# Optimization experiments

Hardware: AMD Instinct MI355X
Metric: run time of the kernel (lower is better)

Reference implementation:

```python
import jax, jax.numpy as jnp
import numpy as np

T, B = 2048, 64
E, H = 256, 256
VOCAB = 50257
PAD_ID = 0


def setup_inputs() -> dict:
    key = jax.random.key(0)
    ks = jax.random.split(key, 9)
    s = 0.05
    return {
        "sentences": jax.random.randint(ks[0], (T, B), 0, VOCAB, dtype=jnp.int64 if jax.config.jax_enable_x64 else jnp.int32),
        "noise": jax.random.uniform(ks[1], (T, B), dtype=jnp.float32),
        "emb": jax.random.normal(ks[2], (VOCAB, E), dtype=jnp.float32) * s,
        "W_ih": jax.random.normal(ks[3], (4 * H, E), dtype=jnp.float32) * s,
        "W_hh": jax.random.normal(ks[4], (4 * H, H), dtype=jnp.float32) * s,
        "b_ih": jax.random.normal(ks[5], (4 * H,), dtype=jnp.float32) * s,
        "b_hh": jax.random.normal(ks[6], (4 * H,), dtype=jnp.float32) * s,
        "W_z": jax.random.normal(ks[7], (H,), dtype=jnp.float32) * s,
        "b_z": jax.random.normal(ks[8], (), dtype=jnp.float32) * s,
    }


def _lstm(x, W_ih, W_hh, b_ih, b_hh):
    # x: (T, B, E) -> hidden states (T, B, H). PyTorch gate order: i, f, g, o.
    Hd = W_hh.shape[1]
    h0 = jnp.zeros((x.shape[1], Hd), x.dtype)
    c0 = jnp.zeros((x.shape[1], Hd), x.dtype)
    b = b_ih + b_hh

    def step(carry, x_t):
        h, c = carry
        g = x_t @ W_ih.T + h @ W_hh.T + b  # (B, 4H)
        i, f, gg, o = jnp.split(g, 4, axis=-1)
        c = jax.nn.sigmoid(f) * c + jax.nn.sigmoid(i) * jnp.tanh(gg)
        h = jax.nn.sigmoid(o) * jnp.tanh(c)
        return (h, c), h

    _, hs = jax.lax.scan(step, (h0, c0), x)
    return hs


def reference(sentences, noise, emb, W_ih, W_hh, b_ih, b_hh, W_z, b_z):
    x = emb[sentences]                         # (T, B, E) embedding gather
    hs = _lstm(x, W_ih, W_hh, b_ih, b_hh)      # (T, B, H)
    pz = jax.nn.sigmoid(jnp.einsum("tbh,h->tb", hs, W_z) + b_z)  # (T, B)
    z = (noise < pz).astype(pz.dtype)          # Bernoulli sample via uniform noise
    z_sizes = z.sum(axis=0).astype(jnp.int32)  # (B,)
    # Stream compaction per column: stable sort brings z==1 positions first,
    # preserving original token order (parallel equivalent of masked_select loop).
    order = jnp.argsort((1.0 - z).astype(jnp.int32), axis=0, stable=True)  # (T, B)
    selected = jnp.take_along_axis(sentences, order.astype(sentences.dtype), axis=0)
    pos = jnp.arange(sentences.shape[0])[:, None]
    rationales = jnp.where(pos < z_sizes[None, :], selected,
                           jnp.asarray(PAD_ID, sentences.dtype))
    return (pz, z, rationales, z_sizes)
```

## Files before the change

### kernel.cpp

```cpp
#include <hip/hip_runtime.h>
#include <math.h>

#define TT 2048
#define NB 64
#define EE 256
#define HH 256
#define PJ 16
#define XLD 288
#define RS1 280
#define RS2 72
#define RBOFF (8 * RS1)

typedef float f32x4 __attribute__((ext_vector_type(4)));

__device__ __forceinline__ float sigf(float x) { return 1.f / (1.f + expf(-x)); }

__device__ __forceinline__ unsigned long long packh(unsigned tag, float v) {
    union { float f; unsigned u; } c; c.f = v;
    return ((unsigned long long)tag << 32) | (unsigned long long)c.u;
}

__global__ __launch_bounds__(512, 2)
void lstm_kernel(const int* __restrict__ sent, const float* __restrict__ emb,
                 const float* __restrict__ W_ih, const float* __restrict__ W_hh,
                 const float* __restrict__ b_ih, const float* __restrict__ b_hh,
                 const float* __restrict__ W_z,
                 unsigned long long* __restrict__ hbuf,
                 float* __restrict__ part)
{
    __shared__ __align__(16) float x_sw[4 * XLD];
    __shared__ __align__(16) float h_sw[4 * XLD];
    __shared__ __align__(16) float red_s[2 * 8 * RS1];
    __shared__ __align__(16) float p_s[64];
    extern __shared__ float dyn_pad[];

    const int tid  = threadIdx.x;
    if (tid == 0 && sent[0] < 0) ((volatile float*)dyn_pad)[0] = 0.f;

    const int xcd  = blockIdx.x & 7;
    const int slot = blockIdx.x >> 3;
    const int psys = xcd * 2 + (slot >> 4);
    const int js   = slot & 15;
    const int bA0  = psys * 2;
    const int bB0  = 32 + psys * 2;
    const int j0   = js * 16;

    const int wv    = tid >> 6;
    const int lane  = tid & 63;
    const int bp    = wv & 1;
    const int kc    = (wv >> 1) * 2 + (lane & 1);
    const int rg    = lane >> 1;
    const int kbase = kc << 5;

    float4 wih_r[16], whh_r[16];
    #pragma unroll
    for (int i = 0; i < 2; ++i) {
        int lr = rg * 2 + i;
        long grow = (long)((lr >> 4) * HH + j0 + (lr & 15));
        const float4* wi = (const float4*)(W_ih + grow * EE + kbase);
        const float4* wh = (const float4*)(W_hh + grow * EE + kbase);
        #pragma unroll
        for (int mi = 0; mi < 8; ++mi) {
            wih_r[i * 8 + mi] = wi[mi];
            whh_r[i * 8 + mi] = wh[mi];
        }
    }

    const int eb  = (lane >> 4) & 1;
    const int ejj = lane & 15;
    float bias_g[4]; float wz_r = 0.f; float c_reg = 0.f;
    if (wv < 2) {
        #pragma unroll
        for (int g = 0; g < 4; ++g)
            bias_g[g] = b_ih[g * HH + j0 + ejj] + b_hh[g * HH + j0 + ejj];
        wz_r = W_z[j0 + ejj];
    }

    const bool spinA = (wv < 4);
    const bool spinB = (wv >= 4);
    const int sidx = ((wv & 3) << 6) + lane;
    const int scb  = sidx >> 7;
    const int scw  = (sidx & 127) << 1;
    const int scph = scw + ((scw >> 5) << 2);

    const bool stgA = (wv == 4 || wv == 5);
    const int srow  = (wv >= 6 ? 2 : 0) + bp;
    const int sphys = 4 * lane + ((lane >> 3) << 2);
    int tok_st = 0;

    if (wv >= 4) {
        int base = stgA ? bA0 : bB0;
        int tk0 = sent[0 * NB + base + bp];
        f32x4 xv0 = ((const f32x4*)(emb + (long)tk0 * EE))[lane];
        *(f32x4*)(&x_sw[srow * XLD + sphys]) = xv0;
        tok_st = sent[1 * NB + base + bp];
    }
    __syncthreads();

    for (int t = 0; t < TT; ++t) {
        const bool pf = (t + 1 < TT);
        const size_t parIn  = (size_t)(((t - 1) & 1) * NB);
        const size_t parOut = (size_t)((t & 1) * NB);
        const unsigned want = (unsigned)t;

        f32x4 xst;
        if (wv >= 4 && pf) {
            xst = ((const f32x4*)(emb + (long)tok_st * EE))[lane];
            if (t + 2 < TT)
                tok_st = sent[(t + 2) * NB + (stgA ? bA0 : bB0) + bp];
        }
        unsigned long long v0 = 0, v1 = 0;
        unsigned long long* hpA = hbuf + (parIn + bA0 + scb) * HH + scw;
        unsigned long long* hpB = hbuf + (parIn + bB0 + scb) * HH + scw;
        if (t > 0 && spinA) {
            v0 = __hip_atomic_load(hpA + 0, __ATOMIC_RELAXED, __HIP_MEMORY_SCOPE_AGENT);
            v1 = __hip_atomic_load(hpA + 1, __ATOMIC_RELAXED, __HIP_MEMORY_SCOPE_AGENT);
        }

        float4 acc[2];
        acc[0] = make_float4(0.f, 0.f, 0.f, 0.f);
        acc[1] = make_float4(0.f, 0.f, 0.f, 0.f);
        {
            const float* xb = &x_sw[bp * XLD + kc * 36];
            #pragma unroll
            for (int mi = 0; mi < 8; ++mi) {
                float4 xv4 = *(const float4*)(xb + mi * 4);
                #pragma unroll
                for (int i = 0; i < 2; ++i) {
                    float4 w = wih_r[i * 8 + mi];
                    acc[i].x += w.x * xv4.x; acc[i].y += w.y * xv4.y;
                    acc[i].z += w.z * xv4.z; acc[i].w += w.w * xv4.w;
                }
            }
        }
        if (t > 0 && spinA) {
            while ((unsigned)(v0 >> 32) != want)
                v0 = __hip_atomic_load(hpA + 0, __ATOMIC_RELAXED, __HIP_MEMORY_SCOPE_AGENT);
            while ((unsigned)(v1 >> 32) != want)
                v1 = __hip_atomic_load(hpA + 1, __ATOMIC_RELAXED, __HIP_MEMORY_SCOPE_AGENT);
            union { unsigned u; float f; } c0, c1;
            c0.u = (unsigned)v0; c1.u = (unsigned)v1;
            *(float2*)(&h_sw[scb * XLD + scph]) = make_float2(c0.f, c1.f);
        }
        __syncthreads();

        if (t > 0 && wv == 2 && lane < 2) {
            float s = 0.f;
            #pragma unroll
            for (int jj = 0; jj < 16; ++jj) s += p_s[lane * 16 + jj];
            part[((size_t)(t - 1) * PJ + js) * NB + bA0 + lane] = s;
        }
        if (t > 0 && spinB) {
            v0 = __hip_atomic_load(hpB + 0, __ATOMIC_RELAXED, __HIP_MEMORY_SCOPE_AGENT);
            v1 = __hip_atomic_load(hpB + 1, __ATOMIC_RELAXED, __HIP_MEMORY_SCOPE_AGENT);
        }
        if (t > 0) {
            const float* hb = &h_sw[bp * XLD + kc * 36];
            #pragma unroll
            for (int mi = 0; mi < 8; ++mi) {
                float4 hv4 = *(const float4*)(hb + mi * 4);
                #pragma unroll
                for (int i = 0; i < 2; ++i) {
                    float4 w = whh_r[i * 8 + mi];
                    acc[i].x += w.x * hv4.x; acc[i].y += w.y * hv4.y;
                    acc[i].z += w.z * hv4.z; acc[i].w += w.w * hv4.w;
                }
            }
        }
        {
            float2 v;
            v.x = (acc[0].x + acc[0].y) + (acc[0].z + acc[0].w);
            v.y = (acc[1].x + acc[1].y) + (acc[1].z + acc[1].w);
            *(float2*)(&red_s[kc * RS1 + bp * RS2 + rg * 2]) = v;
        }
        if (stgA && pf) {
            *(f32x4*)(&x_sw[srow * XLD + sphys]) = xst;
        }
        __syncthreads();

        if (wv == 0 && lane < 32) {
            float sg[4];
            #pragma unroll
            for (int g = 0; g < 4; ++g) {
                float s = bias_g[g];
                #pragma unroll
                for (int k2 = 0; k2 < 8; ++k2)
                    s += red_s[k2 * RS1 + eb * RS2 + g * 16 + ejj];
                sg[g] = s;
            }
            float cn = sigf(sg[1]) * c_reg + sigf(sg[0]) * tanhf(sg[2]);
            float hn = sigf(sg[3]) * tanhf(cn);
            c_reg = cn;
            p_s[lane] = hn * wz_r;
            __hip_atomic_store(
                hbuf + (parOut + bA0 + eb) * HH + j0 + ejj,
                packh((unsigned)(t + 1), hn),
                __ATOMIC_RELAXED, __HIP_MEMORY_SCOPE_AGENT);
        }

        acc[0] = make_float4(0.f, 0.f, 0.f, 0.f);
        acc[1] = make_float4(0.f, 0.f, 0.f, 0.f);
        {
            const float* xb = &x_sw[(2 + bp) * XLD + kc * 36];
            #pragma unroll
            for (int mi = 0; mi < 8; ++mi) {
                float4 xv4 = *(const float4*)(xb + mi * 4);
                #pragma unroll
                for (int i = 0; i < 2; ++i) {
                    float4 w = wih_r[i * 8 + mi];
                    acc[i].x += w.x * xv4.x; acc[i].y += w.y * xv4.y;
                    acc[i].z += w.z * xv4.z; acc[i].w += w.w * xv4.w;
                }
            }
        }
        if (t > 0 && spinB) {
            while ((unsigned)(v0 >> 32) != want)
                v0 = __hip_atomic_load(hpB + 0, __ATOMIC_RELAXED, __HIP_MEMORY_SCOPE_AGENT);
            while ((unsigned)(v1 >> 32) != want)
                v1 = __hip_atomic_load(hpB + 1, __ATOMIC_RELAXED, __HIP_MEMORY_SCOPE_AGENT);
            union { unsigned u; float f; } c0, c1;
            c0.u = (unsigned)v0; c1.u = (unsigned)v1;
            *(float2*)(&h_sw[(2 + scb) * XLD + scph]) = make_float2(c0.f, c1.f);
        }
        __syncthreads();

        if (t > 0 && wv == 3 && lane < 2) {
            float s = 0.f;
            #pragma unroll
            for (int jj = 0; jj < 16; ++jj) s += p_s[32 + lane * 16 + jj];
            part[((size_t)(t - 1) * PJ + js) * NB + bB0 + lane] = s;
        }
        if (t > 0) {
            const float* hb = &h_sw[(2 + bp) * XLD + kc * 36];
            #pragma unroll
            for (int mi = 0; mi < 8; ++mi) {
                float4 hv4 = *(const float4*)(hb + mi * 4);
                #pragma unroll
                for (int i = 0; i < 2; ++i) {
                    float4 w = whh_r[i * 8 + mi];
                    acc[i].x += w.x * hv4.x; acc[i].y += w.y * hv4.y;
                    acc[i].z += w.z * hv4.z; acc[i].w += w.w * hv4.w;
                }
            }
        }
        {
            float2 v;
            v.x = (acc[0].x + acc[0].y) + (acc[0].z + acc[0].w);
            v.y = (acc[1].x + acc[1].y) + (acc[1].z + acc[1].w);
            *(float2*)(&red_s[RBOFF + kc * RS1 + bp * RS2 + rg * 2]) = v;
        }
        if (!stgA && wv >= 4 && pf) {
            *(f32x4*)(&x_sw[srow * XLD + sphys]) = xst;
        }
        __syncthreads();

        if (wv == 1 && lane < 32) {
            float sg[4];
            #pragma unroll
            for (int g = 0; g < 4; ++g) {
                float s = bias_g[g];
                #pragma unroll
                for (int k2 = 0; k2 < 8; ++k2)
                    s += red_s[RBOFF + k2 * RS1 + eb * RS2 + g * 16 + ejj];
                sg[g] = s;
            }
            float cn = sigf(sg[1]) * c_reg + sigf(sg[0]) * tanhf(sg[2]);
            float hn = sigf(sg[3]) * tanhf(cn);
            c_reg = cn;
            p_s[32 + lane] = hn * wz_r;
            __hip_atomic_store(
                hbuf + (parOut + bB0 + eb) * HH + j0 + ejj,
                packh((unsigned)(t + 1), hn),
                __ATOMIC_RELAXED, __HIP_MEMORY_SCOPE_AGENT);
        }
    }

    __syncthreads();
    if (wv == 2 && lane < 2) {
        float s = 0.f;
        #pragma unroll
        for (int jj = 0; jj < 16; ++jj) s += p_s[lane * 16 + jj];
        part[((size_t)(TT - 1) * PJ + js) * NB + bA0 + lane] = s;
    }
    if (wv == 3 && lane < 2) {
        float s = 0.f;
        #pragma unroll
        for (int jj = 0; jj < 16; ++jj) s += p_s[32 + lane * 16 + jj];
        part[((size_t)(TT - 1) * PJ + js) * NB + bB0 + lane] = s;
    }
}

__global__ void pz_kernel(const float* __restrict__ part,
                          const float* __restrict__ noise,
                          const float* __restrict__ b_z,
                          float* __restrict__ out)
{
    int idx = blockIdx.x * blockDim.x + threadIdx.x;
    if (idx >= TT * NB) return;
    int t = idx >> 6, b = idx & 63;
    float s = b_z[0];
    #pragma unroll
    for (int jg = 0; jg < PJ; ++jg) s += part[(t * PJ + jg) * NB + b];
    float pz = 1.f / (1.f + expf(-s));
    out[idx] = pz;
    out[TT * NB + idx] = (noise[idx] < pz) ? 1.f : 0.f;
}

__global__ void compact_kernel(const int* __restrict__ sent,
                               const float* __restrict__ zbuf,
                               float* __restrict__ rat,
                               float* __restrict__ zsz)
{
    __shared__ float rat_s[TT];
    __shared__ int scan_s[256];
    int b = blockIdx.x, tid = threadIdx.x;
    int zloc[8];
    int base = tid * 8;
    int c = 0;
    #pragma unroll
    for (int i = 0; i < 8; ++i) {
        zloc[i] = (zbuf[(base + i) * NB + b] != 0.f) ? 1 : 0;
        c += zloc[i];
    }
    scan_s[tid] = c;
    for (int i = tid; i < TT; i += 256) rat_s[i] = 0.f;
    __syncthreads();
    for (int off = 1; off < 256; off <<= 1) {
        int v = scan_s[tid];
        int add = (tid >= off) ? scan_s[tid - off] : 0;
        __syncthreads();
        scan_s[tid] = v + add;
        __syncthreads();
    }
    int total = scan_s[255];
    int pos = scan_s[tid] - c;
    #pragma unroll
    for (int i = 0; i < 8; ++i) {
        if (zloc[i]) { rat_s[pos] = (float)sent[(base + i) * NB + b]; ++pos; }
    }
    __syncthreads();
    for (int i = tid; i < TT; i += 256) rat[i * NB + b] = rat_s[i];
    if (tid == 0) zsz[b] = (float)total;
}

extern "C" void kernel_launch(void* const* d_in, const int* in_sizes, int n_in,
                              void* d_out, int out_size, void* d_ws, size_t ws_size,
                              hipStream_t stream)
{
    const int*   sent  = (const int*)d_in[0];
    const float* noise = (const float*)d_in[1];
    const float* emb   = (const float*)d_in[2];
    const float* W_ih  = (const float*)d_in[3];
    const float* W_hh  = (const float*)d_in[4];
    const float* b_ih  = (const float*)d_in[5];
    const float* b_hh  = (const float*)d_in[6];
    const float* W_z   = (const float*)d_in[7];
    const float* b_z   = (const float*)d_in[8];
    float* out = (float*)d_out;

    char* ws = (char*)d_ws;
    unsigned long long* hbuf = (unsigned long long*)ws;
    float* part = (float*)(ws + 262144);

    (void)hipMemsetAsync(hbuf, 0, 2 * NB * HH * sizeof(unsigned long long), stream);

    lstm_kernel<<<256, 512, 65536, stream>>>(sent, emb, W_ih, W_hh, b_ih, b_hh,
                                             W_z, hbuf, part);
    pz_kernel<<<(TT * NB) / 256, 256, 0, stream>>>(part, noise, b_z, out);
    compact_kernel<<<NB, 256, 0, stream>>>(sent, out + TT * NB,
                                           out + 2 * TT * NB, out + 3 * TT * NB);
}
```

Baseline: 5.281 ms.

## Remove mid-phase barriers by having each wave poll its own hidden slice

Each wave now spin-loads only the h values it consumes (its kc slice for its batch row) and writes them into its own region of shared memory, so the separate poll-then-__syncthreads stage before each recurrent matvec is removed. This cuts the per-step barrier count from four to two. The B-group embedding staging buffer is double-buffered by timestep parity so it can be written without an extra barrier. The trade-off is that every wave now waits on remote atomics, and each wave issues scalar per-lane polls and shared stores instead of the earlier float2 pattern.

New measurement: 4.288 ms. 1.23x faster.

```diff
diff --git a/kernel.cpp b/kernel.cpp
--- a/kernel.cpp
+++ b/kernel.cpp
@@ -28,7 +28,7 @@
                  unsigned long long* __restrict__ hbuf,
                  float* __restrict__ part)
 {
-    __shared__ __align__(16) float x_sw[4 * XLD];
+    __shared__ __align__(16) float x_sw[6 * XLD];
     __shared__ __align__(16) float h_sw[4 * XLD];
     __shared__ __align__(16) float red_s[2 * 8 * RS1];
     __shared__ __align__(16) float p_s[64];
@@ -76,23 +76,20 @@
         wz_r = W_z[j0 + ejj];
     }
 
-    const bool spinA = (wv < 4);
-    const bool spinB = (wv >= 4);
-    const int sidx = ((wv & 3) << 6) + lane;
-    const int scb  = sidx >> 7;
-    const int scw  = (sidx & 127) << 1;
-    const int scph = scw + ((scw >> 5) << 2);
+    const int pj    = (kc << 5) + (lane >> 1);
+    const int pphys = kc * 36 + (lane >> 1);
 
     const bool stgA = (wv == 4 || wv == 5);
-    const int srow  = (wv >= 6 ? 2 : 0) + bp;
+    const bool stgB = (wv == 6 || wv == 7);
     const int sphys = 4 * lane + ((lane >> 3) << 2);
     int tok_st = 0;
 
-    if (wv >= 4) {
+    if (stgA || stgB) {
         int base = stgA ? bA0 : bB0;
         int tk0 = sent[0 * NB + base + bp];
         f32x4 xv0 = ((const f32x4*)(emb + (long)tk0 * EE))[lane];
-        *(f32x4*)(&x_sw[srow * XLD + sphys]) = xv0;
+        int row = stgA ? bp : (2 + bp);
+        *(f32x4*)(&x_sw[row * XLD + sphys]) = xv0;
         tok_st = sent[1 * NB + base + bp];
     }
     __syncthreads();
@@ -104,17 +101,21 @@
         const unsigned want = (unsigned)t;
 
         f32x4 xst;
-        if (wv >= 4 && pf) {
+        if ((stgA || stgB) && pf) {
             xst = ((const f32x4*)(emb + (long)tok_st * EE))[lane];
             if (t + 2 < TT)
                 tok_st = sent[(t + 2) * NB + (stgA ? bA0 : bB0) + bp];
         }
-        unsigned long long v0 = 0, v1 = 0;
-        unsigned long long* hpA = hbuf + (parIn + bA0 + scb) * HH + scw;
-        unsigned long long* hpB = hbuf + (parIn + bB0 + scb) * HH + scw;
-        if (t > 0 && spinA) {
-            v0 = __hip_atomic_load(hpA + 0, __ATOMIC_RELAXED, __HIP_MEMORY_SCOPE_AGENT);
-            v1 = __hip_atomic_load(hpA + 1, __ATOMIC_RELAXED, __HIP_MEMORY_SCOPE_AGENT);
+        unsigned long long* hpA = hbuf + (parIn + bA0 + bp) * HH + pj;
+        unsigned long long pv = 0;
+        if (t > 0)
+            pv = __hip_atomic_load(hpA, __ATOMIC_RELAXED, __HIP_MEMORY_SCOPE_AGENT);
+
+        if (t > 0 && wv == 2 && lane < 2) {
+            float s = 0.f;
+            #pragma unroll
+            for (int jj = 0; jj < 16; ++jj) s += p_s[lane * 16 + jj];
+            part[((size_t)(t - 1) * PJ + js) * NB + bA0 + lane] = s;
         }
 
         float4 acc[2];
@@ -133,28 +134,11 @@
                 }
             }
         }
-        if (t > 0 && spinA) {
-            while ((unsigned)(v0 >> 32) != want)
-                v0 = __hip_atomic_load(hpA + 0, __ATOMIC_RELAXED, __HIP_MEMORY_SCOPE_AGENT);
-            while ((unsigned)(v1 >> 32) != want)
-                v1 = __hip_atomic_load(hpA + 1, __ATOMIC_RELAXED, __HIP_MEMORY_SCOPE_AGENT);
-            union { unsigned u; float f; } c0, c1;
-            c0.u = (unsigned)v0; c1.u = (unsigned)v1;
-            *(float2*)(&h_sw[scb * XLD + scph]) = make_float2(c0.f, c1.f);
-        }
-        __syncthreads();
-
-        if (t > 0 && wv == 2 && lane < 2) {
-            float s = 0.f;
-            #pragma unroll
-            for (int jj = 0; jj < 16; ++jj) s += p_s[lane * 16 + jj];
-            part[((size_t)(t - 1) * PJ + js) * NB + bA0 + lane] = s;
-        }
-        if (t > 0 && spinB) {
-            v0 = __hip_atomic_load(hpB + 0, __ATOMIC_RELAXED, __HIP_MEMORY_SCOPE_AGENT);
-            v1 = __hip_atomic_load(hpB + 1, __ATOMIC_RELAXED, __HIP_MEMORY_SCOPE_AGENT);
-        }
         if (t > 0) {
+            while ((unsigned)(pv >> 32) != want)
+                pv = __hip_atomic_load(hpA, __ATOMIC_RELAXED, __HIP_MEMORY_SCOPE_AGENT);
+            union { unsigned u; float f; } cu; cu.u = (unsigned)pv;
+            h_sw[bp * XLD + pphys] = cu.f;
             const float* hb = &h_sw[bp * XLD + kc * 36];
             #pragma unroll
             for (int mi = 0; mi < 8; ++mi) {
@@ -173,10 +157,12 @@
             v.y = (acc[1].x + acc[1].y) + (acc[1].z + acc[1].w);
             *(float2*)(&red_s[kc * RS1 + bp * RS2 + rg * 2]) = v;
         }
-        if (stgA && pf) {
-            *(f32x4*)(&x_sw[srow * XLD + sphys]) = xst;
-        }
         __syncthreads();
+
+        unsigned long long* hpB = hbuf + (parIn + bB0 + bp) * HH + pj;
+        unsigned long long qv = 0;
+        if (t > 0)
+            qv = __hip_atomic_load(hpB, __ATOMIC_RELAXED, __HIP_MEMORY_SCOPE_AGENT);
 
         if (wv == 0 && lane < 32) {
             float sg[4];
@@ -197,11 +183,17 @@
                 packh((unsigned)(t + 1), hn),
                 __ATOMIC_RELAXED, __HIP_MEMORY_SCOPE_AGENT);
         }
+        if (t > 0 && wv == 3 && lane < 2) {
+            float s = 0.f;
+            #pragma unroll
+            for (int jj = 0; jj < 16; ++jj) s += p_s[32 + lane * 16 + jj];
+            part[((size_t)(t - 1) * PJ + js) * NB + bB0 + lane] = s;
+        }
 
         acc[0] = make_float4(0.f, 0.f, 0.f, 0.f);
         acc[1] = make_float4(0.f, 0.f, 0.f, 0.f);
         {
-            const float* xb = &x_sw[(2 + bp) * XLD + kc * 36];
+            const float* xb = &x_sw[(2 + 2 * (t & 1) + bp) * XLD + kc * 36];
             #pragma unroll
             for (int mi = 0; mi < 8; ++mi) {
                 float4 xv4 = *(const float4*)(xb + mi * 4);
@@ -213,24 +205,11 @@
                 }
             }
         }
-        if (t > 0 && spinB) {
-            while ((unsigned)(v0 >> 32) != want)
-                v0 = __hip_atomic_load(hpB + 0, __ATOMIC_RELAXED, __HIP_MEMORY_SCOPE_AGENT);
-            while ((unsigned)(v1 >> 32) != want)
-                v1 = __hip_atomic_load(hpB + 1, __ATOMIC_RELAXED, __HIP_MEMORY_SCOPE_AGENT);
-            union { unsigned u; float f; } c0, c1;
-            c0.u = (unsigned)v0; c1.u = (unsigned)v1;
-            *(float2*)(&h_sw[(2 + scb) * XLD + scph]) = make_float2(c0.f, c1.f);
-        }
-        __syncthreads();
-
-        if (t > 0 && wv == 3 && lane < 2) {
-            float s = 0.f;
-            #pragma unroll
-            for (int jj = 0; jj < 16; ++jj) s += p_s[32 + lane * 16 + jj];
-            part[((size_t)(t - 1) * PJ + js) * NB + bB0 + lane] = s;
-        }
         if (t > 0) {
+            while ((unsigned)(qv >> 32) != want)
+                qv = __hip_atomic_load(hpB, __ATOMIC_RELAXED, __HIP_MEMORY_SCOPE_AGENT);
+            union { unsigned u; float f; } cu; cu.u = (unsigned)qv;
+            h_sw[(2 + bp) * XLD + pphys] = cu.f;
             const float* hb = &h_sw[(2 + bp) * XLD + kc * 36];
             #pragma unroll
             for (int mi = 0; mi < 8; ++mi) {
@@ -249,9 +228,10 @@
             v.y = (acc[1].x + acc[1].y) + (acc[1].z + acc[1].w);
             *(float2*)(&red_s[RBOFF + kc * RS1 + bp * RS2 + rg * 2]) = v;
         }
-        if (!stgA && wv >= 4 && pf) {
-            *(f32x4*)(&x_sw[srow * XLD + sphys]) = xst;
-        }
+        if (stgA && pf)
+            *(f32x4*)(&x_sw[bp * XLD + sphys]) = xst;
+        if (stgB && pf)
+            *(f32x4*)(&x_sw[(2 + 2 * ((t + 1) & 1) + bp) * XLD + sphys]) = xst;
         __syncthreads();
 
         if (wv == 1 && lane < 32) {
```
